# Performance work log

Hardware: AMD Instinct MI355X
Metric: run time of the kernel (lower is better)

## Reference

```python
import jax, jax.numpy as jnp
import numpy as np


def setup_inputs() -> dict:
    key = jax.random.key(0)
    ks = jax.random.split(key, 6)
    B, S, I, H = 64, 1024, 1024, 1024
    s_i = 1.0 / np.sqrt(I)
    s_h = 1.0 / np.sqrt(H)
    return {
        "x": jax.random.normal(ks[0], (B, S, I), dtype=jnp.float32),
        "h": jax.random.normal(ks[1], (B, H), dtype=jnp.float32),
        "Wih_w": jax.random.uniform(ks[2], (H, I), jnp.float32, -s_i, s_i),
        "Wih_b": jax.random.uniform(ks[3], (H,), jnp.float32, -s_i, s_i),
        "Whh_w": jax.random.uniform(ks[4], (H, H), jnp.float32, -s_h, s_h),
        "Whh_b": jax.random.uniform(ks[5], (H,), jnp.float32, -s_h, s_h),
    }


def reference(x, h, Wih_w, Wih_b, Whh_w, Whh_b):
    # Precompute input projection for all timesteps in one big GEMM:
    # [B,S,I] @ [I,H] -> [B,S,H]
    wx = jnp.einsum("bsi,hi->bsh", x, Wih_w) + Wih_b

    def step(h_t, wx_t):
        # wx_t: [B,H]; recurrent update h = tanh(Wih x + Whh h)
        h_new = jnp.tanh(wx_t + jnp.einsum("bh,gh->bg", h_t, Whh_w) + Whh_b)
        return h_new, h_new

    # scan over seq dim: move to leading axis [S,B,H]
    h_last, ys = jax.lax.scan(step, h, jnp.swapaxes(wx, 0, 1))
    y = jnp.swapaxes(ys, 0, 1)  # [B,S,H]; dropout p=0 => identity
    return (y, h_last)
```

## Files before the change

### kernel.cpp

```cpp
#include <hip/hip_runtime.h>
#include <cmath>

constexpr int B = 64, S = 1024, I = 1024, H = 1024;
constexpr int KSPLIT = 16;

__global__ __launch_bounds__(256) void gemm_nt(
    const float* __restrict__ A, const float* __restrict__ W,
    const float* __restrict__ bias, float* __restrict__ C) {
  __shared__ float As[16][68];
  __shared__ float Bs[16][68];
  const int tid = threadIdx.x;
  const int m0 = blockIdx.y * 64;
  const int n0 = blockIdx.x * 64;
  const int tx = tid & 15;
  const int ty = tid >> 4;
  const int lr = tid >> 2;
  const int lc = (tid & 3) * 4;

  const float* Ap = A + (size_t)(m0 + lr) * I + lc;
  const float* Wp = W + (size_t)(n0 + lr) * I + lc;

  float acc[4][4] = {};
  for (int k0 = 0; k0 < I; k0 += 16) {
    float4 av = *(const float4*)(Ap + k0);
    float4 wv = *(const float4*)(Wp + k0);
    As[lc + 0][lr] = av.x; As[lc + 1][lr] = av.y;
    As[lc + 2][lr] = av.z; As[lc + 3][lr] = av.w;
    Bs[lc + 0][lr] = wv.x; Bs[lc + 1][lr] = wv.y;
    Bs[lc + 2][lr] = wv.z; Bs[lc + 3][lr] = wv.w;
    __syncthreads();
#pragma unroll
    for (int kk = 0; kk < 16; ++kk) {
      float4 a = *(const float4*)&As[kk][ty * 4];
      float4 b = *(const float4*)&Bs[kk][tx * 4];
      float ar[4] = {a.x, a.y, a.z, a.w};
      float br[4] = {b.x, b.y, b.z, b.w};
#pragma unroll
      for (int i = 0; i < 4; ++i)
#pragma unroll
        for (int j = 0; j < 4; ++j) acc[i][j] += ar[i] * br[j];
    }
    __syncthreads();
  }
  float bj[4];
#pragma unroll
  for (int j = 0; j < 4; ++j) bj[j] = bias[n0 + tx * 4 + j];
#pragma unroll
  for (int i = 0; i < 4; ++i) {
    int m = m0 + ty * 4 + i;
    float4 o = make_float4(acc[i][0] + bj[0], acc[i][1] + bj[1],
                           acc[i][2] + bj[2], acc[i][3] + bj[3]);
    *(float4*)&C[(size_t)m * H + n0 + tx * 4] = o;
  }
}

__global__ __launch_bounds__(256) void rnn_step_gemm(
    const float* __restrict__ hprev, long hstride,
    const float* __restrict__ W, float* __restrict__ partial) {
  __shared__ float Ws[64][68];
  __shared__ float Hs[64][68];
  const int tid = threadIdx.x;
  const int g0 = blockIdx.x * 64;
  const int k0 = blockIdx.y * 64;
  const int tx = tid & 15;
  const int ty = tid >> 4;

  {
    const int r = tid >> 4;
    const int c = (tid & 15) * 4;
#pragma unroll
    for (int p = 0; p < 4; ++p) {
      const int rr = r + p * 16;
      float4 wv = *(const float4*)(W + (size_t)(g0 + rr) * H + k0 + c);
      float4 hv = *(const float4*)(hprev + (size_t)rr * hstride + k0 + c);
      Ws[c + 0][rr] = wv.x; Ws[c + 1][rr] = wv.y;
      Ws[c + 2][rr] = wv.z; Ws[c + 3][rr] = wv.w;
      Hs[c + 0][rr] = hv.x; Hs[c + 1][rr] = hv.y;
      Hs[c + 2][rr] = hv.z; Hs[c + 3][rr] = hv.w;
    }
  }
  __syncthreads();

  float acc[4][4] = {};
#pragma unroll 16
  for (int kk = 0; kk < 64; ++kk) {
    float4 hb = *(const float4*)&Hs[kk][ty * 4];
    float4 wb = *(const float4*)&Ws[kk][tx * 4];
    float hr[4] = {hb.x, hb.y, hb.z, hb.w};
    float wr[4] = {wb.x, wb.y, wb.z, wb.w};
#pragma unroll
    for (int i = 0; i < 4; ++i)
#pragma unroll
      for (int j = 0; j < 4; ++j) acc[i][j] += hr[i] * wr[j];
  }

#pragma unroll
  for (int i = 0; i < 4; ++i) {
    const int b = ty * 4 + i;
    float4 o = make_float4(acc[i][0], acc[i][1], acc[i][2], acc[i][3]);
    *(float4*)&partial[((size_t)blockIdx.y * B + b) * H + g0 + tx * 4] = o;
  }
}

__global__ __launch_bounds__(256) void rnn_finalize(
    const float* __restrict__ partial, const float* __restrict__ bias,
    float* __restrict__ yx, long ystride, float* __restrict__ hlast) {
  const int idx = blockIdx.x * 256 + threadIdx.x;
  const int b = idx >> 10;
  const int g = idx & 1023;
  float v = yx[(size_t)b * ystride + g] + bias[g];
#pragma unroll
  for (int ks = 0; ks < KSPLIT; ++ks)
    v += partial[((size_t)ks * B + b) * H + g];
  v = tanhf(v);
  yx[(size_t)b * ystride + g] = v;
  if (hlast) hlast[idx] = v;
}

extern "C" void kernel_launch(void* const* d_in, const int* in_sizes, int n_in,
                              void* d_out, int out_size, void* d_ws, size_t ws_size,
                              hipStream_t stream) {
  const float* x     = (const float*)d_in[0];
  const float* h0    = (const float*)d_in[1];
  const float* Wih_w = (const float*)d_in[2];
  const float* Wih_b = (const float*)d_in[3];
  const float* Whh_w = (const float*)d_in[4];
  const float* Whh_b = (const float*)d_in[5];

  float* y     = (float*)d_out;
  float* hlast = y + (size_t)B * S * H;
  float* partial = (float*)d_ws;

  gemm_nt<<<dim3(H / 64, (B * S) / 64), 256, 0, stream>>>(x, Wih_w, Wih_b, y);

  for (int t = 0; t < S; ++t) {
    const float* hprev = (t == 0) ? h0 : (y + (size_t)(t - 1) * H);
    const long hstride = (t == 0) ? (long)H : (long)S * H;
    rnn_step_gemm<<<dim3(H / 64, KSPLIT), 256, 0, stream>>>(
        hprev, hstride, Whh_w, partial);
    rnn_finalize<<<256, 256, 0, stream>>>(
        partial, Whh_b, y + (size_t)t * H, (long)S * H,
        (t == S - 1) ? hlast : nullptr);
  }
}
```

Baseline: 11.99 ms.

## Replace per-timestep kernel launches with a persistent cooperative scan kernel

Replaces the 2048 small per-step launches (split-K GEMM plus finalize) with one persistent cooperative kernel of 256 blocks. Each block keeps its 16-row slice of Whh resident in shared memory and computes a 16x16 output tile per step. Steps are separated by a grid-wide barrier built on device-scope atomic counters. This removes launch overhead and the partial-sum round trip through global memory, but relies on the spin barrier and on co-residency of all blocks, and it keeps the old loop as a fallback if the cooperative launch fails.

```diff
diff --git a/kernel.cpp b/kernel.cpp
--- a/kernel.cpp
+++ b/kernel.cpp
@@ -54,17 +54,118 @@
   }
 }
 
+constexpr int SCAN_BLOCKS  = 256;
+constexpr int SCAN_THREADS = 1024;
+constexpr int LP = 1028;
+constexpr int SMEM_FLOATS = 2 * 16 * LP + 3 * 256;
+constexpr size_t SMEM_BYTES = (size_t)SMEM_FLOATS * sizeof(float);
+
+__global__ __launch_bounds__(SCAN_THREADS) void rnn_scan(
+    const float* __restrict__ h0, const float* __restrict__ Whh,
+    const float* __restrict__ bias, float* __restrict__ y,
+    float* __restrict__ hlast, unsigned* __restrict__ bar) {
+  extern __shared__ float smem[];
+  float* Ws  = smem;
+  float* Hs  = smem + 16 * LP;
+  float* red = smem + 32 * LP;
+
+  const int tid = threadIdx.x;
+  const int blk = blockIdx.x;
+  const int g0 = (blk & 63) * 16;
+  const int b0 = (blk >> 6) * 16;
+  const int out = tid & 255;
+  const int tx  = out & 15;
+  const int ty  = out >> 4;
+  const int kq  = tid >> 8;
+  const int kbase = kq * 256;
+
+#pragma unroll
+  for (int p = 0; p < 4; ++p) {
+    const int fidx = p * SCAN_THREADS + tid;
+    const int r = fidx >> 8;
+    const int c = (fidx & 255) * 4;
+    const float4 v = *(const float4*)(Whh + (size_t)(g0 + r) * H + c);
+    *(float4*)&Ws[r * LP + c] = v;
+  }
+  const float bj = bias[g0 + tx];
+  const float* hrow = &Hs[ty * LP + kbase];
+  const float* wrow = &Ws[tx * LP + kbase];
+
+  for (int t = 0; t < S; ++t) {
+    const float* hp = (t == 0) ? (h0 + (size_t)b0 * H)
+                               : (y + ((size_t)b0 * S + (t - 1)) * H);
+    const size_t hstr = (t == 0) ? (size_t)H : (size_t)S * H;
+#pragma unroll
+    for (int p = 0; p < 4; ++p) {
+      const int fidx = p * SCAN_THREADS + tid;
+      const int r = fidx >> 8;
+      const int c = (fidx & 255) * 4;
+      const float4 v = *(const float4*)(hp + (size_t)r * hstr + c);
+      *(float4*)&Hs[r * LP + c] = v;
+    }
+    float* yp = &y[((size_t)(b0 + ty) * S + t) * H + g0 + tx];
+    const float wx = (kq == 0) ? *yp : 0.f;
+    __syncthreads();
+
+    float a0 = 0.f, a1 = 0.f, a2 = 0.f, a3 = 0.f;
+#pragma unroll
+    for (int k = 0; k < 256; k += 16) {
+      float4 h0v = *(const float4*)(hrow + k + 0);
+      float4 w0v = *(const float4*)(wrow + k + 0);
+      float4 h1v = *(const float4*)(hrow + k + 4);
+      float4 w1v = *(const float4*)(wrow + k + 4);
+      float4 h2v = *(const float4*)(hrow + k + 8);
+      float4 w2v = *(const float4*)(wrow + k + 8);
+      float4 h3v = *(const float4*)(hrow + k + 12);
+      float4 w3v = *(const float4*)(wrow + k + 12);
+      a0 = fmaf(h0v.x, w0v.x, a0); a0 = fmaf(h0v.y, w0v.y, a0);
+      a0 = fmaf(h0v.z, w0v.z, a0); a0 = fmaf(h0v.w, w0v.w, a0);
+      a1 = fmaf(h1v.x, w1v.x, a1); a1 = fmaf(h1v.y, w1v.y, a1);
+      a1 = fmaf(h1v.z, w1v.z, a1); a1 = fmaf(h1v.w, w1v.w, a1);
+      a2 = fmaf(h2v.x, w2v.x, a2); a2 = fmaf(h2v.y, w2v.y, a2);
+      a2 = fmaf(h2v.z, w2v.z, a2); a2 = fmaf(h2v.w, w2v.w, a2);
+      a3 = fmaf(h3v.x, w3v.x, a3); a3 = fmaf(h3v.y, w3v.y, a3);
+      a3 = fmaf(h3v.z, w3v.z, a3); a3 = fmaf(h3v.w, w3v.w, a3);
+    }
+    float acc = (a0 + a1) + (a2 + a3);
+    if (kq != 0) red[(kq - 1) * 256 + out] = acc;
+    __syncthreads();
+    if (kq == 0) {
+      acc += red[out] + red[256 + out] + red[512 + out];
+      const float v = tanhf(wx + bj + acc);
+      *yp = v;
+      if (t == S - 1) hlast[(size_t)(b0 + ty) * H + g0 + tx] = v;
+    }
+
+    if (t != S - 1) {
+      __builtin_amdgcn_fence(__ATOMIC_RELEASE, "workgroup");
+      __syncthreads();
+      if (tid == 0) {
+        __builtin_amdgcn_fence(__ATOMIC_RELEASE, "agent");
+        __hip_atomic_fetch_add(&bar[(blk & 3) * 64], 1u, __ATOMIC_RELAXED,
+                               __HIP_MEMORY_SCOPE_AGENT);
+        const unsigned tgt = (unsigned)(t + 1) * 64u;
+#pragma unroll 1
+        for (int c = 0; c < 4; ++c)
+          while (__hip_atomic_load(&bar[c * 64], __ATOMIC_RELAXED,
+                                   __HIP_MEMORY_SCOPE_AGENT) < tgt) { }
+        __builtin_amdgcn_fence(__ATOMIC_ACQUIRE, "agent");
+      }
+      __syncthreads();
+    }
+  }
+}
+
 __global__ __launch_bounds__(256) void rnn_step_gemm(
     const float* __restrict__ hprev, long hstride,
     const float* __restrict__ W, float* __restrict__ partial) {
-  __shared__ float Ws[64][68];
-  __shared__ float Hs[64][68];
+  __shared__ float Wsm[64][68];
+  __shared__ float Hsm[64][68];
   const int tid = threadIdx.x;
   const int g0 = blockIdx.x * 64;
   const int k0 = blockIdx.y * 64;
   const int tx = tid & 15;
   const int ty = tid >> 4;
-
   {
     const int r = tid >> 4;
     const int c = (tid & 15) * 4;
@@ -73,19 +174,18 @@
       const int rr = r + p * 16;
       float4 wv = *(const float4*)(W + (size_t)(g0 + rr) * H + k0 + c);
       float4 hv = *(const float4*)(hprev + (size_t)rr * hstride + k0 + c);
-      Ws[c + 0][rr] = wv.x; Ws[c + 1][rr] = wv.y;
-      Ws[c + 2][rr] = wv.z; Ws[c + 3][rr] = wv.w;
-      Hs[c + 0][rr] = hv.x; Hs[c + 1][rr] = hv.y;
-      Hs[c + 2][rr] = hv.z; Hs[c + 3][rr] = hv.w;
+      Wsm[c + 0][rr] = wv.x; Wsm[c + 1][rr] = wv.y;
+      Wsm[c + 2][rr] = wv.z; Wsm[c + 3][rr] = wv.w;
+      Hsm[c + 0][rr] = hv.x; Hsm[c + 1][rr] = hv.y;
+      Hsm[c + 2][rr] = hv.z; Hsm[c + 3][rr] = hv.w;
     }
   }
   __syncthreads();
-
   float acc[4][4] = {};
 #pragma unroll 16
   for (int kk = 0; kk < 64; ++kk) {
-    float4 hb = *(const float4*)&Hs[kk][ty * 4];
-    float4 wb = *(const float4*)&Ws[kk][tx * 4];
+    float4 hb = *(const float4*)&Hsm[kk][ty * 4];
+    float4 wb = *(const float4*)&Wsm[kk][tx * 4];
     float hr[4] = {hb.x, hb.y, hb.z, hb.w};
     float wr[4] = {wb.x, wb.y, wb.z, wb.w};
 #pragma unroll
@@ -93,7 +193,6 @@
 #pragma unroll
       for (int j = 0; j < 4; ++j) acc[i][j] += hr[i] * wr[j];
   }
-
 #pragma unroll
   for (int i = 0; i < 4; ++i) {
     const int b = ty * 4 + i;
@@ -129,17 +228,37 @@
 
   float* y     = (float*)d_out;
   float* hlast = y + (size_t)B * S * H;
-  float* partial = (float*)d_ws;
+  unsigned* bar = (unsigned*)d_ws;
+
+  hipMemsetAsync(bar, 0, 4 * 64 * sizeof(unsigned), stream);
 
   gemm_nt<<<dim3(H / 64, (B * S) / 64), 256, 0, stream>>>(x, Wih_w, Wih_b, y);
 
-  for (int t = 0; t < S; ++t) {
-    const float* hprev = (t == 0) ? h0 : (y + (size_t)(t - 1) * H);
-    const long hstride = (t == 0) ? (long)H : (long)S * H;
-    rnn_step_gemm<<<dim3(H / 64, KSPLIT), 256, 0, stream>>>(
-        hprev, hstride, Whh_w, partial);
-    rnn_finalize<<<256, 256, 0, stream>>>(
-        partial, Whh_b, y + (size_t)t * H, (long)S * H,
-        (t == S - 1) ? hlast : nullptr);
-  }
-}
+  static bool attr_done = false;
+  if (!attr_done) {
+    hipFuncSetAttribute((const void*)rnn_scan,
+                        hipFuncAttributeMaxDynamicSharedMemorySize,
+                        (int)SMEM_BYTES);
+    attr_done = true;
+  }
+
+  const float* a_h0 = h0; const float* a_W = Whh_w; const float* a_b = Whh_b;
+  float* a_y = y; float* a_hl = hlast; unsigned* a_bar = bar;
+  void* args[] = {&a_h0, &a_W, &a_b, &a_y, &a_hl, &a_bar};
+  hipError_t ce = hipLaunchCooperativeKernel(
+      (const void*)rnn_scan, dim3(SCAN_BLOCKS), dim3(SCAN_THREADS), args,
+      (unsigned)SMEM_BYTES, stream);
+
+  if (ce != hipSuccess) {
+    float* partial = (float*)d_ws + 256;
+    for (int t = 0; t < S; ++t) {
+      const float* hprev = (t == 0) ? h0 : (y + (size_t)(t - 1) * H);
+      const long hstride = (t == 0) ? (long)H : (long)S * H;
+      rnn_step_gemm<<<dim3(H / 64, KSPLIT), 256, 0, stream>>>(
+          hprev, hstride, Whh_w, partial);
+      rnn_finalize<<<256, 256, 0, stream>>>(
+          partial, Whh_b, y + (size_t)t * H, (long)S * H,
+          (t == S - 1) ? hlast : nullptr);
+    }
+  }
+}
```

Measured after the change: 18.36 ms. 53.2% more time.
